# Kernel optimization log

Hardware: AMD Instinct MI355X
Metric: run time of the kernel (lower is better)

Reference implementation:

```python
import jax, jax.numpy as jnp
import numpy as np
import math

INPUT_SIZE = 1024
HIDDEN_SIZE = 1024
RANK = 256
BATCH = 32
SEQ = 512


def setup_inputs() -> dict:
    key = jax.random.key(0)
    k_x, k_a, k_b, k_c = jax.random.split(key, 4)
    stdv = 1.0 / math.sqrt(HIDDEN_SIZE)
    x = jax.random.normal(k_x, (BATCH, SEQ, INPUT_SIZE), dtype=jnp.float32)
    a = jax.random.uniform(k_a, (HIDDEN_SIZE, RANK * 4), minval=-stdv, maxval=stdv, dtype=jnp.float32)
    b = jax.random.uniform(k_b, (INPUT_SIZE, RANK * 4), minval=-stdv, maxval=stdv, dtype=jnp.float32)
    ct = jax.random.uniform(k_c, (RANK * 4, HIDDEN_SIZE), minval=-stdv, maxval=stdv, dtype=jnp.float32)
    return {"x": x, "a": a, "b": b, "ct": ct}


def reference(x, a, b, ct):
    B, S, _ = x.shape
    H = a.shape[0]
    R = a.shape[1] // 4
    ct3 = ct.reshape(4, R, H)  # (4, R, H)
    # Precompute input projection for all timesteps: (B, S, 4R)
    xb = jnp.einsum('bsi,ir->bsr', x, b)

    def step(carry, xb_t):
        h, c = carry
        g = (h @ a) * xb_t                      # (B, 4R)
        g = jnp.einsum('bkr,krh->bkh', g.reshape(B, 4, R), ct3)  # (B, 4, H)
        f_t = jax.nn.sigmoid(g[:, 0])
        i_t = jax.nn.sigmoid(g[:, 1])
        g_t = jnp.tanh(g[:, 2])
        o_t = jax.nn.sigmoid(g[:, 3])
        c = f_t * c + i_t * g_t
        h = o_t * jnp.tanh(c)
        return (h, c), h

    h0 = jnp.zeros((B, H), dtype=x.dtype)
    c0 = jnp.zeros((B, H), dtype=x.dtype)
    (h_t, c_t), hs = jax.lax.scan(step, (h0, c0), jnp.swapaxes(xb, 0, 1))
    hidden_seq = jnp.swapaxes(hs, 0, 1)  # (B, S, H)
    return hidden_seq, (h_t, c_t)
```

## Files before the change

### kernel.cpp

```cpp
#include <hip/hip_runtime.h>
#include <math.h>

#define NTHR 512

__device__ __forceinline__ void st_uc(float* p, float v) {
    asm volatile("global_store_dword %0, %1, off sc0 sc1" :: "v"(p), "v"(v) : "memory");
}

__global__ void init_kernel(float* bufs, unsigned* flags) {
    int i = blockIdx.x * blockDim.x + threadIdx.x;
    if (i < 65536) bufs[i] = 0.0f;
    if (i < 4096) flags[i] = 0u;
}

__global__ __launch_bounds__(256) void xb_gemm(const float* __restrict__ X,
                                               const float* __restrict__ Bw,
                                               float* __restrict__ XB) {
    __shared__ float xs[16][132];
    __shared__ float bs[16][132];
    const int bm = blockIdx.x >> 3;
    const int bn = blockIdx.x & 7;
    const int m0 = bm * 128, n0 = bn * 128;
    const int tid = threadIdx.x;
    const int tx = tid & 15, ty = tid >> 4;
    float acc[8][8];
#pragma unroll
    for (int i = 0; i < 8; ++i)
#pragma unroll
        for (int j = 0; j < 8; ++j) acc[i][j] = 0.f;

    for (int k0 = 0; k0 < 1024; k0 += 16) {
#pragma unroll
        for (int p = 0; p < 2; ++p) {
            int f = tid + p * 256;
            int m = f >> 2, kq = f & 3;
            float4 v = *(const float4*)&X[(size_t)(m0 + m) * 1024 + k0 + kq * 4];
            xs[kq * 4 + 0][m] = v.x; xs[kq * 4 + 1][m] = v.y;
            xs[kq * 4 + 2][m] = v.z; xs[kq * 4 + 3][m] = v.w;
        }
#pragma unroll
        for (int p = 0; p < 2; ++p) {
            int f = tid + p * 256;
            int k = f >> 5, n = (f & 31) * 4;
            float4 v = *(const float4*)&Bw[(size_t)(k0 + k) * 1024 + n0 + n];
            *(float4*)&bs[k][n] = v;
        }
        __syncthreads();
#pragma unroll
        for (int k = 0; k < 16; ++k) {
            float xv[8], bv[8];
            *(float4*)&xv[0] = *(const float4*)&xs[k][ty * 8];
            *(float4*)&xv[4] = *(const float4*)&xs[k][ty * 8 + 4];
            *(float4*)&bv[0] = *(const float4*)&bs[k][tx * 8];
            *(float4*)&bv[4] = *(const float4*)&bs[k][tx * 8 + 4];
#pragma unroll
            for (int i = 0; i < 8; ++i)
#pragma unroll
                for (int j = 0; j < 8; ++j) acc[i][j] += xv[i] * bv[j];
        }
        __syncthreads();
    }
#pragma unroll
    for (int i = 0; i < 8; ++i)
#pragma unroll
        for (int j = 0; j < 8; j += 4) {
            float4 v = make_float4(acc[i][j], acc[i][j + 1], acc[i][j + 2], acc[i][j + 3]);
            *(float4*)&XB[(size_t)(m0 + ty * 8 + i) * 1024 + n0 + tx * 8 + j] = v;
        }
}

__device__ __forceinline__ void group_barrier(unsigned* gf, int sub, int tid, unsigned bar) {
    asm volatile("s_waitcnt vmcnt(0)" ::: "memory");
    __syncthreads();
    if (tid == 0) {
        bool last = false;
        unsigned a = __hip_atomic_fetch_add(gf + (sub << 5), 1u, __ATOMIC_RELAXED, __HIP_MEMORY_SCOPE_AGENT);
        if (a == bar * 8u - 1u) {
            unsigned b = __hip_atomic_fetch_add(gf + 256, 1u, __ATOMIC_RELAXED, __HIP_MEMORY_SCOPE_AGENT);
            if (b == bar * 8u - 1u) {
                __hip_atomic_store(gf + 288, bar, __ATOMIC_RELAXED, __HIP_MEMORY_SCOPE_AGENT);
                last = true;
            }
        }
        if (!last) {
            while (__hip_atomic_load(gf + 288, __ATOMIC_RELAXED, __HIP_MEMORY_SCOPE_AGENT) < bar)
                __builtin_amdgcn_s_sleep(1);
        }
    }
    __syncthreads();
}

__global__ __launch_bounds__(NTHR, 1) void scan_kernel(
    const float* __restrict__ A, const float* __restrict__ CTm,
    float* __restrict__ XBH, float* __restrict__ h_buf, float* __restrict__ g_buf,
    float* __restrict__ ht_out, float* __restrict__ ct_out, unsigned* flags) {
    extern __shared__ float lds[];
    float* a_lf  = lds;
    float* ct_lf = lds + 16384;
    float* hg_f  = lds + 32768;
    float4* a_l4  = (float4*)a_lf;
    float4* ct_l4 = (float4*)ct_lf;
    float4* hg_4  = (float4*)hg_f;
    float* scr = hg_f;

    const int wg = blockIdx.x;
    const int bg = wg >> 6;
    const int sg = wg & 63;
    const int c0wg = sg * 16;
    const int tid = threadIdx.x;
    unsigned* gf = flags + (bg << 10);
    const int sub = sg >> 3;

    {
        const int c = tid & 15, i0 = tid >> 4;
        for (int i = i0; i < 1024; i += 32) {
            a_lf[c * 1024 + i]  = A[(size_t)i * 1024 + c0wg + c];
            ct_lf[c * 1024 + i] = CTm[(size_t)i * 1024 + c0wg + c];
        }
    }

    const int L  = tid & 63;
    const int w  = tid >> 6;
    const int Lc = L & 7;
    const int Lb = (L >> 3) & 7;
    const int cgA = w & 1, kqA = w >> 1;
    const int gB  = w >> 1;

    int hIdx[8], aIdx[8], gIdx[8], cIdx[8];
#pragma unroll
    for (int r = 0; r < 8; ++r) hIdx[r] = (r ^ Lb) * 256 + kqA * 64 + L;
#pragma unroll
    for (int c = 0; c < 8; ++c) aIdx[c] = (cgA * 8 + (c ^ Lc)) * 256 + kqA * 64 + L;
#pragma unroll
    for (int r = 0; r < 8; ++r) gIdx[r] = (r ^ Lb) * 256 + gB * 64 + L;
#pragma unroll
    for (int c = 0; c < 8; ++c) cIdx[c] = (cgA * 8 + (c ^ Lc)) * 256 + gB * 64 + L;

    const int e_b  = tid >> 4;
    const int e_j  = tid & 15;
    const int e_cg = e_j >> 3;
    const int e_slot = e_b * 8 + (e_j & 7);
    const int e_bglob = bg * 8 + e_b;
    const int e_col   = c0wg + e_j;

    const float4* hsrc4 = (const float4*)(h_buf + (size_t)bg * 8192);
    const float4* gsrc4 = (const float4*)(g_buf + (size_t)bg * 8192);

    float creg = 0.f;
    unsigned barc = 0;
    __syncthreads();

    for (int t = 0; t < 512; ++t) {
        float xbv = 0.f;
        if (tid < 128) xbv = XBH[((size_t)e_bglob * 512 + t) * 1024 + e_col];

        {
            float4 v0, v1, v2, v3;
            asm volatile("global_load_dwordx4 %0, %1, off sc0 sc1" : "=v"(v0) : "v"(hsrc4 + tid) : "memory");
            asm volatile("global_load_dwordx4 %0, %1, off sc0 sc1" : "=v"(v1) : "v"(hsrc4 + 512 + tid) : "memory");
            asm volatile("global_load_dwordx4 %0, %1, off sc0 sc1" : "=v"(v2) : "v"(hsrc4 + 1024 + tid) : "memory");
            asm volatile("global_load_dwordx4 %0, %1, off sc0 sc1" : "=v"(v3) : "v"(hsrc4 + 1536 + tid) : "memory");
            asm volatile("s_waitcnt vmcnt(0)" ::: "memory");
            __builtin_amdgcn_sched_barrier(0);
            hg_4[tid] = v0; hg_4[512 + tid] = v1; hg_4[1024 + tid] = v2; hg_4[1536 + tid] = v3;
            __syncthreads();
        }
        float v[64];
        {
            float4 hv[8], av[8];
#pragma unroll
            for (int r = 0; r < 8; ++r) hv[r] = hg_4[hIdx[r]];
#pragma unroll
            for (int c = 0; c < 8; ++c) av[c] = a_l4[aIdx[c]];
#pragma unroll
            for (int r = 0; r < 8; ++r)
#pragma unroll
                for (int c = 0; c < 8; ++c)
                    v[r * 8 + c] = hv[r].x * av[c].x + hv[r].y * av[c].y
                                 + hv[r].z * av[c].z + hv[r].w * av[c].w;
        }
#pragma unroll
        for (int j = 0; j < 32; ++j) v[j] = v[2 * j] + __shfl_xor(v[2 * j + 1], 1);
#pragma unroll
        for (int j = 0; j < 16; ++j) v[j] = v[2 * j] + __shfl_xor(v[2 * j + 1], 2);
#pragma unroll
        for (int j = 0; j < 8; ++j)  v[j] = v[2 * j] + __shfl_xor(v[2 * j + 1], 4);
#pragma unroll
        for (int j = 0; j < 4; ++j)  v[j] = v[2 * j] + __shfl_xor(v[2 * j + 1], 8);
#pragma unroll
        for (int j = 0; j < 2; ++j)  v[j] = v[2 * j] + __shfl_xor(v[2 * j + 1], 16);
        v[0] = v[0] + __shfl_xor(v[1], 32);

        __syncthreads();
        scr[w * 64 + L] = v[0];
        __syncthreads();
        if (tid < 128) {
            float s = scr[(0 * 2 + e_cg) * 64 + e_slot] + scr[(1 * 2 + e_cg) * 64 + e_slot]
                    + scr[(2 * 2 + e_cg) * 64 + e_slot] + scr[(3 * 2 + e_cg) * 64 + e_slot];
            st_uc(g_buf + (size_t)e_bglob * 1024 + e_col, s * xbv);
        }
        group_barrier(gf, sub, tid, ++barc);

        {
            float4 v0, v1, v2, v3;
            asm volatile("global_load_dwordx4 %0, %1, off sc0 sc1" : "=v"(v0) : "v"(gsrc4 + tid) : "memory");
            asm volatile("global_load_dwordx4 %0, %1, off sc0 sc1" : "=v"(v1) : "v"(gsrc4 + 512 + tid) : "memory");
            asm volatile("global_load_dwordx4 %0, %1, off sc0 sc1" : "=v"(v2) : "v"(gsrc4 + 1024 + tid) : "memory");
            asm volatile("global_load_dwordx4 %0, %1, off sc0 sc1" : "=v"(v3) : "v"(gsrc4 + 1536 + tid) : "memory");
            asm volatile("s_waitcnt vmcnt(0)" ::: "memory");
            __builtin_amdgcn_sched_barrier(0);
            hg_4[tid] = v0; hg_4[512 + tid] = v1; hg_4[1024 + tid] = v2; hg_4[1536 + tid] = v3;
            __syncthreads();
        }
        {
            float4 gv[8], cv[8];
#pragma unroll
            for (int r = 0; r < 8; ++r) gv[r] = hg_4[gIdx[r]];
#pragma unroll
            for (int c = 0; c < 8; ++c) cv[c] = ct_l4[cIdx[c]];
#pragma unroll
            for (int r = 0; r < 8; ++r)
#pragma unroll
                for (int c = 0; c < 8; ++c)
                    v[r * 8 + c] = gv[r].x * cv[c].x + gv[r].y * cv[c].y
                                 + gv[r].z * cv[c].z + gv[r].w * cv[c].w;
        }
#pragma unroll
        for (int j = 0; j < 32; ++j) v[j] = v[2 * j] + __shfl_xor(v[2 * j + 1], 1);
#pragma unroll
        for (int j = 0; j < 16; ++j) v[j] = v[2 * j] + __shfl_xor(v[2 * j + 1], 2);
#pragma unroll
        for (int j = 0; j < 8; ++j)  v[j] = v[2 * j] + __shfl_xor(v[2 * j + 1], 4);
#pragma unroll
        for (int j = 0; j < 4; ++j)  v[j] = v[2 * j] + __shfl_xor(v[2 * j + 1], 8);
#pragma unroll
        for (int j = 0; j < 2; ++j)  v[j] = v[2 * j] + __shfl_xor(v[2 * j + 1], 16);
        v[0] = v[0] + __shfl_xor(v[1], 32);

        __syncthreads();
        scr[w * 64 + L] = v[0];
        __syncthreads();
        if (tid < 128) {
            float pf = scr[(0 * 2 + e_cg) * 64 + e_slot];
            float pi = scr[(1 * 2 + e_cg) * 64 + e_slot];
            float pg = scr[(2 * 2 + e_cg) * 64 + e_slot];
            float po = scr[(3 * 2 + e_cg) * 64 + e_slot];
            float ft = 1.f / (1.f + __expf(-pf));
            float it = 1.f / (1.f + __expf(-pi));
            float gt = tanhf(pg);
            float ot = 1.f / (1.f + __expf(-po));
            creg = ft * creg + it * gt;
            float hv2 = ot * tanhf(creg);
            st_uc(h_buf + (size_t)e_bglob * 1024 + e_col, hv2);
            st_uc(XBH + ((size_t)e_bglob * 512 + t) * 1024 + e_col, hv2);
            if (t == 511) {
                st_uc(ht_out + (size_t)e_bglob * 1024 + e_col, hv2);
                st_uc(ct_out + (size_t)e_bglob * 1024 + e_col, creg);
            }
        }
        group_barrier(gf, sub, tid, ++barc);
    }
}

extern "C" void kernel_launch(void* const* d_in, const int* in_sizes, int n_in,
                              void* d_out, int out_size, void* d_ws, size_t ws_size,
                              hipStream_t stream) {
    const float* X   = (const float*)d_in[0];
    const float* A   = (const float*)d_in[1];
    const float* Bw  = (const float*)d_in[2];
    const float* CTm = (const float*)d_in[3];

    float* out    = (float*)d_out;
    float* XBH    = out;
    float* ht_out = out + (size_t)32 * 512 * 1024;
    float* ct_out = ht_out + 32 * 1024;

    float* h_buf = (float*)d_ws;
    float* g_buf = h_buf + 32 * 1024;
    unsigned* flags = (unsigned*)(g_buf + 32 * 1024);

    (void)hipFuncSetAttribute((const void*)scan_kernel,
                              hipFuncAttributeMaxDynamicSharedMemorySize, 163840);

    init_kernel<<<dim3(256), dim3(256), 0, stream>>>(h_buf, flags);
    xb_gemm<<<dim3(1024), dim3(256), 0, stream>>>(X, Bw, XBH);
    scan_kernel<<<dim3(256), dim3(NTHR), 163840, stream>>>(A, CTm, XBH, h_buf, g_buf,
                                                           ht_out, ct_out, flags);
}
```

Measured before the change: 5.307 ms.

## Replace hierarchical atomic barrier with per-workgroup tag flags and double buffers

Removes the two-level atomic counter barrier between the h and g phases. Each workgroup now publishes a monotonically increasing tag after writing its slice, and each consumer spins only on the tags of the producers it reads. h and g buffers are double-buffered by timestep parity so a fast producer does not overwrite data a slow reader still needs. Epilogue work is moved onto wave 0, with each lane handling two batch rows. The catch is that many threads now poll uncached flag loads.

```diff
diff --git a/kernel.cpp b/kernel.cpp
--- a/kernel.cpp
+++ b/kernel.cpp
@@ -6,11 +6,26 @@
 __device__ __forceinline__ void st_uc(float* p, float v) {
     asm volatile("global_store_dword %0, %1, off sc0 sc1" :: "v"(p), "v"(v) : "memory");
 }
-
-__global__ void init_kernel(float* bufs, unsigned* flags) {
+__device__ __forceinline__ void st_uc_u(unsigned* p, unsigned v) {
+    asm volatile("global_store_dword %0, %1, off sc0 sc1" :: "v"(p), "v"(v) : "memory");
+}
+__device__ __forceinline__ float4 ld_uc4(const float4* p) {
+    float4 v;
+    asm volatile("global_load_dwordx4 %0, %1, off sc0 sc1" : "=v"(v) : "v"(p) : "memory");
+    return v;
+}
+__device__ __forceinline__ void spin_tag(const unsigned* p, unsigned target) {
+    unsigned v;
+    do {
+        asm volatile("global_load_dword %0, %1, off sc0 sc1\n\ts_waitcnt vmcnt(0)"
+                     : "=v"(v) : "v"(p) : "memory");
+    } while (v < target);
+}
+
+__global__ void init_kernel(float* h_buf, unsigned* tags) {
     int i = blockIdx.x * blockDim.x + threadIdx.x;
-    if (i < 65536) bufs[i] = 0.0f;
-    if (i < 4096) flags[i] = 0u;
+    if (i < 65536) st_uc(h_buf + i, 0.0f);
+    if (i < 512) st_uc_u(tags + i, 0u);
 }
 
 __global__ __launch_bounds__(256) void xb_gemm(const float* __restrict__ X,
@@ -69,31 +84,10 @@
         }
 }
 
-__device__ __forceinline__ void group_barrier(unsigned* gf, int sub, int tid, unsigned bar) {
-    asm volatile("s_waitcnt vmcnt(0)" ::: "memory");
-    __syncthreads();
-    if (tid == 0) {
-        bool last = false;
-        unsigned a = __hip_atomic_fetch_add(gf + (sub << 5), 1u, __ATOMIC_RELAXED, __HIP_MEMORY_SCOPE_AGENT);
-        if (a == bar * 8u - 1u) {
-            unsigned b = __hip_atomic_fetch_add(gf + 256, 1u, __ATOMIC_RELAXED, __HIP_MEMORY_SCOPE_AGENT);
-            if (b == bar * 8u - 1u) {
-                __hip_atomic_store(gf + 288, bar, __ATOMIC_RELAXED, __HIP_MEMORY_SCOPE_AGENT);
-                last = true;
-            }
-        }
-        if (!last) {
-            while (__hip_atomic_load(gf + 288, __ATOMIC_RELAXED, __HIP_MEMORY_SCOPE_AGENT) < bar)
-                __builtin_amdgcn_s_sleep(1);
-        }
-    }
-    __syncthreads();
-}
-
 __global__ __launch_bounds__(NTHR, 1) void scan_kernel(
     const float* __restrict__ A, const float* __restrict__ CTm,
     float* __restrict__ XBH, float* __restrict__ h_buf, float* __restrict__ g_buf,
-    float* __restrict__ ht_out, float* __restrict__ ct_out, unsigned* flags) {
+    float* __restrict__ ht_out, float* __restrict__ ct_out, unsigned* __restrict__ tags) {
     extern __shared__ float lds[];
     float* a_lf  = lds;
     float* ct_lf = lds + 16384;
@@ -108,8 +102,8 @@
     const int sg = wg & 63;
     const int c0wg = sg * 16;
     const int tid = threadIdx.x;
-    unsigned* gf = flags + (bg << 10);
-    const int sub = sg >> 3;
+    unsigned* tagH = tags + (bg << 7);
+    unsigned* tagG = tagH + 64;
 
     {
         const int c = tid & 15, i0 = tid >> 4;
@@ -136,35 +130,42 @@
 #pragma unroll
     for (int c = 0; c < 8; ++c) cIdx[c] = (cgA * 8 + (c ^ Lc)) * 256 + gB * 64 + L;
 
-    const int e_b  = tid >> 4;
-    const int e_j  = tid & 15;
+    const int jneed = (tid >> 2) & 63;
+
+    const int e_b0 = L >> 4;
+    const int e_j  = L & 15;
     const int e_cg = e_j >> 3;
-    const int e_slot = e_b * 8 + (e_j & 7);
-    const int e_bglob = bg * 8 + e_b;
-    const int e_col   = c0wg + e_j;
-
-    const float4* hsrc4 = (const float4*)(h_buf + (size_t)bg * 8192);
-    const float4* gsrc4 = (const float4*)(g_buf + (size_t)bg * 8192);
-
-    float creg = 0.f;
-    unsigned barc = 0;
+    const int e_s0 = e_b0 * 8 + (e_j & 7);
+    const int e_s1 = (e_b0 + 4) * 8 + (e_j & 7);
+    const int bglob0 = bg * 8 + e_b0;
+    const int bglob1 = bglob0 + 4;
+    const int e_col  = c0wg + e_j;
+
+    float4* h4 = (float4*)h_buf;
+    float4* g4 = (float4*)g_buf;
+
+    float creg0 = 0.f, creg1 = 0.f;
     __syncthreads();
 
     for (int t = 0; t < 512; ++t) {
-        float xbv = 0.f;
-        if (tid < 128) xbv = XBH[((size_t)e_bglob * 512 + t) * 1024 + e_col];
-
+        const unsigned tu = (unsigned)t;
+        spin_tag(tagH + jneed, tu);
         {
-            float4 v0, v1, v2, v3;
-            asm volatile("global_load_dwordx4 %0, %1, off sc0 sc1" : "=v"(v0) : "v"(hsrc4 + tid) : "memory");
-            asm volatile("global_load_dwordx4 %0, %1, off sc0 sc1" : "=v"(v1) : "v"(hsrc4 + 512 + tid) : "memory");
-            asm volatile("global_load_dwordx4 %0, %1, off sc0 sc1" : "=v"(v2) : "v"(hsrc4 + 1024 + tid) : "memory");
-            asm volatile("global_load_dwordx4 %0, %1, off sc0 sc1" : "=v"(v3) : "v"(hsrc4 + 1536 + tid) : "memory");
+            const float4* hb = h4 + ((t + 1) & 1) * 8192 + bg * 2048;
+            float4 v0 = ld_uc4(hb + tid);
+            float4 v1 = ld_uc4(hb + 512 + tid);
+            float4 v2 = ld_uc4(hb + 1024 + tid);
+            float4 v3 = ld_uc4(hb + 1536 + tid);
             asm volatile("s_waitcnt vmcnt(0)" ::: "memory");
             __builtin_amdgcn_sched_barrier(0);
             hg_4[tid] = v0; hg_4[512 + tid] = v1; hg_4[1024 + tid] = v2; hg_4[1536 + tid] = v3;
             __syncthreads();
         }
+        float xb0 = 0.f, xb1 = 0.f;
+        if (w == 0) {
+            xb0 = XBH[((size_t)bglob0 * 512 + t) * 1024 + e_col];
+            xb1 = XBH[((size_t)bglob1 * 512 + t) * 1024 + e_col];
+        }
         float v[64];
         {
             float4 hv[8], av[8];
@@ -194,19 +195,30 @@
         __syncthreads();
         scr[w * 64 + L] = v[0];
         __syncthreads();
-        if (tid < 128) {
-            float s = scr[(0 * 2 + e_cg) * 64 + e_slot] + scr[(1 * 2 + e_cg) * 64 + e_slot]
-                    + scr[(2 * 2 + e_cg) * 64 + e_slot] + scr[(3 * 2 + e_cg) * 64 + e_slot];
-            st_uc(g_buf + (size_t)e_bglob * 1024 + e_col, s * xbv);
-        }
-        group_barrier(gf, sub, tid, ++barc);
-
+        float sA0 = 0.f, sA1 = 0.f;
+        if (w == 0) {
+#pragma unroll
+            for (int kq = 0; kq < 4; ++kq) {
+                sA0 += scr[(kq * 2 + e_cg) * 64 + e_s0];
+                sA1 += scr[(kq * 2 + e_cg) * 64 + e_s1];
+            }
+        }
+        __syncthreads();
+        if (w == 0) {
+            float* gw = g_buf + (t & 1) * 32768;
+            st_uc(gw + (size_t)bglob0 * 1024 + e_col, sA0 * xb0);
+            st_uc(gw + (size_t)bglob1 * 1024 + e_col, sA1 * xb1);
+            asm volatile("s_waitcnt vmcnt(0)" ::: "memory");
+            if (L == 0) st_uc_u(tagG + sg, tu + 1u);
+        }
+
+        spin_tag(tagG + jneed, tu + 1u);
         {
-            float4 v0, v1, v2, v3;
-            asm volatile("global_load_dwordx4 %0, %1, off sc0 sc1" : "=v"(v0) : "v"(gsrc4 + tid) : "memory");
-            asm volatile("global_load_dwordx4 %0, %1, off sc0 sc1" : "=v"(v1) : "v"(gsrc4 + 512 + tid) : "memory");
-            asm volatile("global_load_dwordx4 %0, %1, off sc0 sc1" : "=v"(v2) : "v"(gsrc4 + 1024 + tid) : "memory");
-            asm volatile("global_load_dwordx4 %0, %1, off sc0 sc1" : "=v"(v3) : "v"(gsrc4 + 1536 + tid) : "memory");
+            const float4* gb = g4 + (t & 1) * 8192 + bg * 2048;
+            float4 v0 = ld_uc4(gb + tid);
+            float4 v1 = ld_uc4(gb + 512 + tid);
+            float4 v2 = ld_uc4(gb + 1024 + tid);
+            float4 v3 = ld_uc4(gb + 1536 + tid);
             asm volatile("s_waitcnt vmcnt(0)" ::: "memory");
             __builtin_amdgcn_sched_barrier(0);
             hg_4[tid] = v0; hg_4[512 + tid] = v1; hg_4[1024 + tid] = v2; hg_4[1536 + tid] = v3;
@@ -240,25 +252,42 @@
         __syncthreads();
         scr[w * 64 + L] = v[0];
         __syncthreads();
-        if (tid < 128) {
-            float pf = scr[(0 * 2 + e_cg) * 64 + e_slot];
-            float pi = scr[(1 * 2 + e_cg) * 64 + e_slot];
-            float pg = scr[(2 * 2 + e_cg) * 64 + e_slot];
-            float po = scr[(3 * 2 + e_cg) * 64 + e_slot];
-            float ft = 1.f / (1.f + __expf(-pf));
-            float it = 1.f / (1.f + __expf(-pi));
-            float gt = tanhf(pg);
-            float ot = 1.f / (1.f + __expf(-po));
-            creg = ft * creg + it * gt;
-            float hv2 = ot * tanhf(creg);
-            st_uc(h_buf + (size_t)e_bglob * 1024 + e_col, hv2);
-            st_uc(XBH + ((size_t)e_bglob * 512 + t) * 1024 + e_col, hv2);
+        float pf0 = 0.f, pi0 = 0.f, pg0 = 0.f, po0 = 0.f;
+        float pf1 = 0.f, pi1 = 0.f, pg1 = 0.f, po1 = 0.f;
+        if (w == 0) {
+            pf0 = scr[(0 + e_cg) * 64 + e_s0]; pi0 = scr[(2 + e_cg) * 64 + e_s0];
+            pg0 = scr[(4 + e_cg) * 64 + e_s0]; po0 = scr[(6 + e_cg) * 64 + e_s0];
+            pf1 = scr[(0 + e_cg) * 64 + e_s1]; pi1 = scr[(2 + e_cg) * 64 + e_s1];
+            pg1 = scr[(4 + e_cg) * 64 + e_s1]; po1 = scr[(6 + e_cg) * 64 + e_s1];
+        }
+        __syncthreads();
+        if (w == 0) {
+            float ft = 1.f / (1.f + __expf(-pf0));
+            float it = 1.f / (1.f + __expf(-pi0));
+            float gt = tanhf(pg0);
+            float ot = 1.f / (1.f + __expf(-po0));
+            creg0 = ft * creg0 + it * gt;
+            float hv0 = ot * tanhf(creg0);
+            ft = 1.f / (1.f + __expf(-pf1));
+            it = 1.f / (1.f + __expf(-pi1));
+            gt = tanhf(pg1);
+            ot = 1.f / (1.f + __expf(-po1));
+            creg1 = ft * creg1 + it * gt;
+            float hv1 = ot * tanhf(creg1);
+            float* hw = h_buf + (t & 1) * 32768;
+            st_uc(hw + (size_t)bglob0 * 1024 + e_col, hv0);
+            st_uc(hw + (size_t)bglob1 * 1024 + e_col, hv1);
+            st_uc(XBH + ((size_t)bglob0 * 512 + t) * 1024 + e_col, hv0);
+            st_uc(XBH + ((size_t)bglob1 * 512 + t) * 1024 + e_col, hv1);
             if (t == 511) {
-                st_uc(ht_out + (size_t)e_bglob * 1024 + e_col, hv2);
-                st_uc(ct_out + (size_t)e_bglob * 1024 + e_col, creg);
+                st_uc(ht_out + (size_t)bglob0 * 1024 + e_col, hv0);
+                st_uc(ht_out + (size_t)bglob1 * 1024 + e_col, hv1);
+                st_uc(ct_out + (size_t)bglob0 * 1024 + e_col, creg0);
+                st_uc(ct_out + (size_t)bglob1 * 1024 + e_col, creg1);
             }
-        }
-        group_barrier(gf, sub, tid, ++barc);
+            asm volatile("s_waitcnt vmcnt(0)" ::: "memory");
+            if (L == 0) st_uc_u(tagH + sg, tu + 1u);
+        }
     }
 }
 
@@ -276,14 +305,14 @@
     float* ct_out = ht_out + 32 * 1024;
 
     float* h_buf = (float*)d_ws;
-    float* g_buf = h_buf + 32 * 1024;
-    unsigned* flags = (unsigned*)(g_buf + 32 * 1024);
+    float* g_buf = h_buf + 65536;
+    unsigned* tags = (unsigned*)(g_buf + 65536);
 
     (void)hipFuncSetAttribute((const void*)scan_kernel,
                               hipFuncAttributeMaxDynamicSharedMemorySize, 163840);
 
-    init_kernel<<<dim3(256), dim3(256), 0, stream>>>(h_buf, flags);
+    init_kernel<<<dim3(256), dim3(256), 0, stream>>>(h_buf, tags);
     xb_gemm<<<dim3(1024), dim3(256), 0, stream>>>(X, Bw, XBH);
     scan_kernel<<<dim3(256), dim3(NTHR), 163840, stream>>>(A, CTm, XBH, h_buf, g_buf,
-                                                           ht_out, ct_out, flags);
-}
+                                                           ht_out, ct_out, tags);
+}
```

Result: slower. 7.653 ms (+44.2%).
